# Kernel optimization log

Measured on AMD Instinct MI355X. Metric: run time of the kernel, lower is better.

Reference implementation:

```python
import jax, jax.numpy as jnp
import numpy as np

THRESHOLD = 1e-4


def setup_inputs() -> dict:
    key = jax.random.key(0)
    k1, k2, k3, k4 = jax.random.split(key, 4)
    B, C, T = 512, 128, 1000
    D, O = 64, 4
    X = jax.random.normal(k1, (B, C, T), dtype=jnp.float32)
    # Stiefel-initialized bilinear map W: [1, C, D] with orthonormal columns
    W0 = jax.random.uniform(k2, (1, C, D), dtype=jnp.float32)
    s, U = jnp.linalg.eigh(jnp.swapaxes(W0, -1, -2) @ W0)
    A = (U * jax.lax.rsqrt(jnp.clip(s, THRESHOLD, None))[..., None, :]) @ jnp.swapaxes(U, -1, -2)
    W = W0 @ A
    lin_w = jax.random.normal(k3, (O, D * D), dtype=jnp.float32) / np.sqrt(D * D)
    lin_b = jax.random.normal(k4, (O,), dtype=jnp.float32) * 0.01
    return {"X": X, "W": W, "lin_w": lin_w, "lin_b": lin_b}


def reference(X, W, lin_w, lin_b):
    # CovLayer: per-sample covariance over time axis, correction=0
    T = X.shape[-1]
    Xc = X - jnp.mean(X, axis=-1, keepdims=True)          # [B, C, T]
    Cov = jnp.einsum('bct,bdt->bcd', Xc, Xc) / T           # [B, C, C]
    # BiMap: W^T X W  (W broadcasts over batch)
    Y = jnp.swapaxes(W, -1, -2) @ Cov @ W                  # [B, D, D]
    # ReEig: clamp eigenvalues at threshold, recompose
    s, U = jnp.linalg.eigh(Y)
    s = jnp.clip(s, THRESHOLD, None)
    Y = (U * s[..., None, :]) @ jnp.swapaxes(U, -1, -2)
    # LogEig: log eigenvalues, recompose
    s2, U2 = jnp.linalg.eigh(Y)
    Y = (U2 * jnp.log(s2)[..., None, :]) @ jnp.swapaxes(U2, -1, -2)
    # Flatten + Linear classifier (logsoftmax disabled: add_log_softmax=False)
    F = Y.reshape(Y.shape[0], -1)                          # [B, D*D]
    return F @ lin_w.T + lin_b                             # [B, O]
```

## Files before the change

kernel.cpp:

```cpp
#include <hip/hip_runtime.h>
#include <math.h>

#define NDEG 12

typedef unsigned short u16;
typedef unsigned int u32;
typedef _Float16 f16;
typedef __attribute__((ext_vector_type(8))) _Float16 f16x8;
typedef __attribute__((ext_vector_type(8))) short bf16x8;
typedef __attribute__((ext_vector_type(4))) float f32x4;

#define MFMA_F16(a, b, c)  __builtin_amdgcn_mfma_f32_16x16x32_f16(a, b, c, 0, 0, 0)
#define MFMA_BF16(a, b, c) __builtin_amdgcn_mfma_f32_16x16x32_bf16(a, b, c, 0, 0, 0)

__device__ __forceinline__ u32 fbits(float x) { return __float_as_uint(x); }
__device__ __forceinline__ float fval(u32 u) { return __uint_as_float(u); }
__device__ __forceinline__ f32x4 zero4() {
  f32x4 z; z[0] = 0.f; z[1] = 0.f; z[2] = 0.f; z[3] = 0.f; return z;
}
__device__ __forceinline__ u16 f16bits(f16 x) { u16 u; __builtin_memcpy(&u, &x, 2); return u; }
__device__ __forceinline__ float f16tof(u16 u) { f16 h; __builtin_memcpy(&h, &u, 2); return (float)h; }

__device__ __forceinline__ void split2(float x, u32& h, u32& l) {
  u32 u = fbits(x);
  h = u >> 16;
  float lo = x - fval(u & 0xFFFF0000u);
  u32 v = fbits(lo);
  l = (v + 0x7FFFu + ((v >> 16) & 1u)) >> 16;
}
__device__ __forceinline__ void writePair(u32* Hw, u32* Lw, int widx, float v, int lane) {
  float pv = __shfl_xor(v, 1);
  u32 hv, lv, hp, lp;
  split2(v, hv, lv);
  split2(pv, hp, lp);
  const bool even = (lane & 1) == 0;
  u32 word = even ? (hv | (hp << 16)) : (lp | (lv << 16));
  u32* base = even ? Hw : Lw;
  base[widx] = word;
}

struct CovPh { char buf[3][16384]; };
struct ProjPh { u16 Cov[128][136]; u16 Wt[64][136]; };
struct ChebPh {
  u16 MH[64][72]; u16 ML[64][72];
  u16 TbH[2][64][72]; u16 TbL[2][64][72];
};
struct RedPh { float red[256][4]; };
union SmemU { CovPh a; ProjPh p; ChebPh c; RedPh r; };
static_assert(sizeof(SmemU) <= 65536, "smem");

template <int W, int H>
__device__ __forceinline__ void gram8(const char* bufb, int fo0, int fo1,
                                      f32x4 (&acc)[5], f32x4& xs, f16x8 ones) {
  constexpr int I2 = 7 - W;
#pragma unroll
  for (int ch = 0; ch < 2; ++ch) {
    const int fo = ch ? fo1 : fo0;
    const f16x8 Fi1 = *(const f16x8*)(bufb + W * 2048 + fo);
    const f16x8 Fi2 = *(const f16x8*)(bufb + I2 * 2048 + fo);
    const f16x8 Fxs = *(const f16x8*)(bufb + (2 * W + H) * 2048 + fo);
#pragma unroll
    for (int k = 0; k < 9; ++k) {
      if ((k & 1) != H) continue;
      const int I = (k <= 7 - W) ? W : I2;
      const int J = (k <= 7 - W) ? (W + k) : (I2 + (k - (8 - W)));
      const f16x8 Fj = *(const f16x8*)(bufb + J * 2048 + fo);
      acc[k >> 1] = MFMA_F16((I == W) ? Fi1 : Fi2, Fj, acc[k >> 1]);
    }
    xs = MFMA_F16(Fxs, ones, xs);
  }
}

__device__ __forceinline__ void covTile(u16* Cov, const f32x4& v, int I, int J,
                                        int l15, int l16, bool mirror) {
#pragma unroll
  for (int r = 0; r < 4; ++r) {
    int row = 16 * I + 4 * l16 + r;
    int col = 16 * J + l15;
    u16 h = f16bits((f16)(v[r] * 1e-3f));
    Cov[row * 136 + col] = h;
    if (mirror) Cov[col * 136 + row] = h;
  }
}

template <int W, int H>
__device__ __forceinline__ void covStore8(u16* Cov, const f32x4 (&acc)[5], int l15, int l16) {
  constexpr int I2 = 7 - W;
#pragma unroll
  for (int k = 0; k < 9; ++k) {
    if ((k & 1) != H) continue;
    const int I = (k <= 7 - W) ? W : I2;
    const int J = (k <= 7 - W) ? (W + k) : (I2 + (k - (8 - W)));
    covTile(Cov, acc[k >> 1], I, J, l15, l16, I != J);
  }
}

__global__ __launch_bounds__(512, 4) void spdnet_fused9_kernel(
    const float* __restrict__ X, const float* __restrict__ W,
    const float* __restrict__ lin_w, const float* __restrict__ lin_b,
    float* __restrict__ out)
{
  __shared__ SmemU sm;
  __shared__ float mwL[64];
  __shared__ float xsL[128];

  const int tid = threadIdx.x;
  const int lane = tid & 63;
  const int wv = tid >> 6;
  const int l15 = lane & 15;
  const int l16 = lane >> 4;
  const int b = blockIdx.x;
  const char* __restrict__ Xbc = (const char*)(X + (size_t)b * 128000u);

  int goff[4], lb[4];
#pragma unroll
  for (int q = 0; q < 4; ++q) {
    const int rq = 16 * wv + 4 * q + l16;
    goff[q] = rq * 4000 + l15 * 16;
    lb[q] = rq * 128 + ((l15 * 8) ^ ((rq & 7) << 4));
  }
  const int swz = (l15 & 7) << 4;
  const int fo0 = l15 * 128 + ((16 * l16) ^ swz);
  const int fo1 = l15 * 128 + ((16 * l16 + 64) ^ swz);

  f16x8 ones;
#pragma unroll
  for (int i = 0; i < 8; ++i) ones[i] = (f16)1.0f;

  f32x4 acc[5];
#pragma unroll
  for (int u = 0; u < 5; ++u) acc[u] = zero4();
  f32x4 xs = zero4();

  float4 ldA[4], ldB[4];

#define L4(ld, tile)                                              \
  do {                                                            \
    _Pragma("unroll")                                             \
    for (int q = 0; q < 4; ++q)                                   \
      ld[q] = *(const float4*)(Xbc + goff[q] + (tile) * 256);     \
  } while (0)
#define L4_TAIL(ld)                                               \
  do {                                                            \
    const bool valid = l15 < 10;                                  \
    const int off = valid ? 3840 : (3984 - l15 * 16);             \
    _Pragma("unroll")                                             \
    for (int q = 0; q < 4; ++q) {                                 \
      float4 v = *(const float4*)(Xbc + goff[q] + off);           \
      ld[q] = valid ? v : make_float4(0.f, 0.f, 0.f, 0.f);        \
    }                                                             \
  } while (0)
#define S4(bi, ld)                                                \
  do {                                                            \
    char* rb_ = sm.a.buf[bi];                                     \
    _Pragma("unroll")                                             \
    for (int q = 0; q < 4; ++q) {                                 \
      u32 w0 = (u32)f16bits((f16)ld[q].x) | ((u32)f16bits((f16)ld[q].y) << 16); \
      u32 w1 = (u32)f16bits((f16)ld[q].z) | ((u32)f16bits((f16)ld[q].w) << 16); \
      uint2 wr; wr.x = w0; wr.y = w1;                             \
      *(uint2*)(rb_ + lb[q]) = wr;                                \
    }                                                             \
  } while (0)

  auto GRAM = [&](const char* rb) {
    switch (wv) {
      case 0: gram8<0,0>(rb, fo0, fo1, acc, xs, ones); break;
      case 1: gram8<0,1>(rb, fo0, fo1, acc, xs, ones); break;
      case 2: gram8<1,0>(rb, fo0, fo1, acc, xs, ones); break;
      case 3: gram8<1,1>(rb, fo0, fo1, acc, xs, ones); break;
      case 4: gram8<2,0>(rb, fo0, fo1, acc, xs, ones); break;
      case 5: gram8<2,1>(rb, fo0, fo1, acc, xs, ones); break;
      case 6: gram8<3,0>(rb, fo0, fo1, acc, xs, ones); break;
      default: gram8<3,1>(rb, fo0, fo1, acc, xs, ones); break;
    }
  };

  L4(ldA, 0);
  L4(ldB, 1);
  asm volatile("s_waitcnt vmcnt(4)" ::: "memory");
  S4(0, ldA);
  asm volatile("s_waitcnt lgkmcnt(0)" ::: "memory");
  __builtin_amdgcn_s_barrier();

  for (int h = 0; h < 8; ++h) {
    if (h < 7) L4(ldA, 2 * h + 2);
    GRAM(sm.a.buf[(2 * h) % 3]);
    if (h < 7) asm volatile("s_waitcnt vmcnt(4)" ::: "memory");
    else       asm volatile("s_waitcnt vmcnt(0)" ::: "memory");
    S4((2 * h + 1) % 3, ldB);
    asm volatile("s_waitcnt lgkmcnt(0)" ::: "memory");
    __builtin_amdgcn_s_barrier();
    if (h < 6) L4(ldB, 2 * h + 3);
    else if (h == 6) L4_TAIL(ldB);
    GRAM(sm.a.buf[(2 * h + 1) % 3]);
    if (h < 7) {
      asm volatile("s_waitcnt vmcnt(4)" ::: "memory");
      S4((2 * h + 2) % 3, ldA);
      asm volatile("s_waitcnt lgkmcnt(0)" ::: "memory");
      __builtin_amdgcn_s_barrier();
    }
  }
#undef L4
#undef L4_TAIL
#undef S4

  if (l15 == 0) {
#pragma unroll
    for (int r = 0; r < 4; ++r) xsL[16 * wv + 4 * l16 + r] = xs[r];
  }
  __syncthreads();

  {
    u16* CovP = &sm.p.Cov[0][0];
    switch (wv) {
      case 0: covStore8<0,0>(CovP, acc, l15, l16); break;
      case 1: covStore8<0,1>(CovP, acc, l15, l16); break;
      case 2: covStore8<1,0>(CovP, acc, l15, l16); break;
      case 3: covStore8<1,1>(CovP, acc, l15, l16); break;
      case 4: covStore8<2,0>(CovP, acc, l15, l16); break;
      case 5: covStore8<2,1>(CovP, acc, l15, l16); break;
      case 6: covStore8<3,0>(CovP, acc, l15, l16); break;
      default: covStore8<3,1>(CovP, acc, l15, l16); break;
    }
    u16* WtP = &sm.p.Wt[0][0];
    const int c = tid & 127, dh = tid >> 7;
    const float4* wp = (const float4*)(W + c * 64 + 16 * dh);
#pragma unroll
    for (int q = 0; q < 4; ++q) {
      float4 v = wp[q];
      int d0 = 16 * dh + 4 * q;
      WtP[(d0    ) * 136 + c] = f16bits((f16)v.x);
      WtP[(d0 + 1) * 136 + c] = f16bits((f16)v.y);
      WtP[(d0 + 2) * 136 + c] = f16bits((f16)v.z);
      WtP[(d0 + 3) * 136 + c] = f16bits((f16)v.w);
    }
  }
  __syncthreads();

  if (tid < 64) {
    float s = 0.f;
    for (int c = 0; c < 128; ++c)
      s = fmaf(f16tof(sm.p.Wt[tid][c]), xsL[c], s);
    mwL[tid] = s * 1.0e-3f;
  }

  const u16* CovP = &sm.p.Cov[0][0];
  const u16* WtP  = &sm.p.Wt[0][0];
  f32x4 pAcc[4];
#pragma unroll
  for (int n = 0; n < 4; ++n) pAcc[n] = zero4();
#pragma unroll
  for (int ch = 0; ch < 4; ++ch) {
    f16x8 aC = *(const f16x8*)&CovP[(16 * wv + l15) * 136 + 8 * l16 + 32 * ch];
#pragma unroll
    for (int n = 0; n < 4; ++n) {
      f16x8 bw = *(const f16x8*)&WtP[(16 * n + l15) * 136 + 8 * l16 + 32 * ch];
      pAcc[n] = MFMA_F16(aC, bw, pAcc[n]);
    }
  }
  __syncthreads();

  {
    u16* PtP = (u16*)&sm.p.Cov[0][0];
#pragma unroll
    for (int n = 0; n < 4; ++n)
#pragma unroll
      for (int r = 0; r < 4; ++r) {
        int c = 16 * wv + 4 * l16 + r;
        int d = 16 * n + l15;
        PtP[d * 136 + c] = f16bits((f16)pAcc[n][r]);
      }
  }
  __syncthreads();

  const u16* PtP = (const u16*)&sm.p.Cov[0][0];
  f32x4 yAcc[4];
#pragma unroll
  for (int n = 0; n < 4; ++n) yAcc[n] = zero4();
  if (wv < 4) {
#pragma unroll
    for (int ch = 0; ch < 4; ++ch) {
      f16x8 aW = *(const f16x8*)&WtP[(16 * wv + l15) * 136 + 8 * l16 + 32 * ch];
#pragma unroll
      for (int n = 0; n < 4; ++n) {
        f16x8 bP = *(const f16x8*)&PtP[(16 * n + l15) * 136 + 8 * l16 + 32 * ch];
        yAcc[n] = MFMA_F16(aW, bP, yAcc[n]);
      }
    }
  }
  __syncthreads();

  const float CC = 1.125f;
  const float IH = 1.0f / 0.875f;
  const float uu = 0.875f / 1.125f;
  const float rho = (sqrtf(1.0f - uu * uu) - 1.0f) / uu;
  const float a0c = logf(CC / (1.0f + rho * rho));
  const float a1c = -2.0f * rho;

  f32x4 zz[4], tp[4], tcu[4];
  if (wv < 4) {
    u32* MHw = (u32*)&sm.c.MH[0][0];
    u32* MLw = (u32*)&sm.c.ML[0][0];
#pragma unroll
    for (int n = 0; n < 4; ++n)
#pragma unroll
      for (int r = 0; r < 4; ++r) {
        int i = 16 * wv + 4 * l16 + r, j = 16 * n + l15;
        float y = yAcc[n][r] - mwL[i] * mwL[j];
        float m = (y - ((i == j) ? CC : 0.f)) * IH;
        float e = (i == j) ? 1.f : 0.f;
        tp[n][r] = e;
        tcu[n][r] = m;
        zz[n][r] = a0c * e + a1c * m;
        writePair(MHw, MLw, i * 36 + (j >> 1), m, lane);
      }
  }
  __syncthreads();

  bf16x8 aMh[2], aMl[2];
  if (wv < 4) {
#pragma unroll
    for (int ch = 0; ch < 2; ++ch) {
      aMh[ch] = *(const bf16x8*)&sm.c.MH[16 * wv + l15][8 * l16 + 32 * ch];
      aMl[ch] = *(const bf16x8*)&sm.c.ML[16 * wv + l15][8 * l16 + 32 * ch];
    }
  }

  float rhok = rho;
  for (int k = 2; k <= NDEG; ++k) {
    rhok *= rho;
    const float ak = (-2.0f / (float)k) * rhok;
    if (wv < 4) {
      const u16 (*srcH)[72] = (k == 2) ? sm.c.MH : sm.c.TbH[(k - 1) & 1];
      const u16 (*srcL)[72] = (k == 2) ? sm.c.ML : sm.c.TbL[(k - 1) & 1];
      f32x4 p[4];
#pragma unroll
      for (int n = 0; n < 4; ++n) p[n] = zero4();
#pragma unroll
      for (int ch = 0; ch < 2; ++ch) {
#pragma unroll
        for (int n = 0; n < 4; ++n) {
          bf16x8 bh = *(const bf16x8*)&srcH[16 * n + l15][8 * l16 + 32 * ch];
          bf16x8 bl = *(const bf16x8*)&srcL[16 * n + l15][8 * l16 + 32 * ch];
          p[n] = MFMA_BF16(aMh[ch], bh, p[n]);
          p[n] = MFMA_BF16(aMh[ch], bl, p[n]);
          p[n] = MFMA_BF16(aMl[ch], bh, p[n]);
        }
      }
      u32* dH = (u32*)&sm.c.TbH[k & 1][0][0];
      u32* dL = (u32*)&sm.c.TbL[k & 1][0][0];
#pragma unroll
      for (int n = 0; n < 4; ++n) {
        f32x4 tn;
#pragma unroll
        for (int r = 0; r < 4; ++r) {
          tn[r] = 2.f * p[n][r] - tp[n][r];
          zz[n][r] = fmaf(ak, tn[r], zz[n][r]);
        }
        tp[n] = tcu[n];
        tcu[n] = tn;
        if (k < NDEG) {
#pragma unroll
          for (int r = 0; r < 4; ++r) {
            int row = 16 * wv + 4 * l16 + r, col = 16 * n + l15;
            writePair(dH, dL, row * 36 + (col >> 1), tn[r], lane);
          }
        }
      }
    }
    if (k < NDEG) __syncthreads();
  }
  __syncthreads();

  if (wv < 4) {
    float po[4] = {0.f, 0.f, 0.f, 0.f};
#pragma unroll
    for (int n = 0; n < 4; ++n)
#pragma unroll
      for (int r = 0; r < 4; ++r) {
        int i = 16 * wv + 4 * l16 + r, j = 16 * n + l15;
        const float zv = zz[n][r];
        const int base = i * 64 + j;
#pragma unroll
        for (int o = 0; o < 4; ++o)
          po[o] = fmaf(zv, lin_w[o * 4096 + base], po[o]);
      }
#pragma unroll
    for (int o = 0; o < 4; ++o) sm.r.red[tid][o] = po[o];
  }
  __syncthreads();
  if (tid < 64) {
    const int g = tid >> 4, li = tid & 15;
    float s = 0.f;
#pragma unroll
    for (int q = 0; q < 16; ++q) s += sm.r.red[li + 16 * q][g];
#pragma unroll
    for (int d = 8; d >= 1; d >>= 1) s += __shfl_down(s, d);
    if (li == 0) out[b * 4 + g] = s + lin_b[g];
  }
}

extern "C" void kernel_launch(void* const* d_in, const int* in_sizes, int n_in,
                              void* d_out, int out_size, void* d_ws, size_t ws_size,
                              hipStream_t stream) {
  const float* X     = (const float*)d_in[0];
  const float* W     = (const float*)d_in[1];
  const float* lin_w = (const float*)d_in[2];
  const float* lin_b = (const float*)d_in[3];
  float* out = (float*)d_out;
  spdnet_fused9_kernel<<<512, 512, 0, stream>>>(X, W, lin_w, lin_b, out);
}
```

Baseline: 75.72 us.

## Replace triple-buffered small tiles with single 64KB buffer and large batched loads

The covariance stage previously streamed X in 64-column tiles through a triple-buffered LDS ring, with a barrier per tile. It now loads 256 columns per step into 16 registers per thread, fills one 64KB LDS buffer, and runs four gram passes per barrier pair over four phases. This cuts barrier count and issues larger, more coalesced global loads. In exchange it needs more registers (launch bounds drop to 2 waves per SIMD), and it no longer overlaps the LDS store with compute since the single buffer must be drained before refill.

```diff
diff --git a/kernel.cpp b/kernel.cpp
--- a/kernel.cpp
+++ b/kernel.cpp
@@ -39,7 +39,7 @@
   base[widx] = word;
 }
 
-struct CovPh { char buf[3][16384]; };
+struct CovPh { char buf[65536]; };
 struct ProjPh { u16 Cov[128][136]; u16 Wt[64][136]; };
 struct ChebPh {
   u16 MH[64][72]; u16 ML[64][72];
@@ -47,7 +47,7 @@
 };
 struct RedPh { float red[256][4]; };
 union SmemU { CovPh a; ProjPh p; ChebPh c; RedPh r; };
-static_assert(sizeof(SmemU) <= 65536, "smem");
+static_assert(sizeof(SmemU) == 65536, "smem");
 
 template <int W, int H>
 __device__ __forceinline__ void gram8(const char* bufb, int fo0, int fo1,
@@ -95,7 +95,7 @@
   }
 }
 
-__global__ __launch_bounds__(512, 4) void spdnet_fused9_kernel(
+__global__ __launch_bounds__(512, 2) void spdnet_fused11_kernel(
     const float* __restrict__ X, const float* __restrict__ W,
     const float* __restrict__ lin_w, const float* __restrict__ lin_b,
     float* __restrict__ out)
@@ -112,13 +112,13 @@
   const int b = blockIdx.x;
   const char* __restrict__ Xbc = (const char*)(X + (size_t)b * 128000u);
 
-  int goff[4], lb[4];
-#pragma unroll
-  for (int q = 0; q < 4; ++q) {
-    const int rq = 16 * wv + 4 * q + l16;
-    goff[q] = rq * 4000 + l15 * 16;
-    lb[q] = rq * 128 + ((l15 * 8) ^ ((rq & 7) << 4));
-  }
+  int voff[16];
+#pragma unroll
+  for (int q = 0; q < 16; ++q)
+    voff[q] = (16 * wv + q) * 4000 + lane * 16;
+
+  const int sBase = (lane >> 4) * 16384 + wv * 2048;
+  const int w8 = 8 * (lane & 15);
   const int swz = (l15 & 7) << 4;
   const int fo0 = l15 * 128 + ((16 * l16) ^ swz);
   const int fo1 = l15 * 128 + ((16 * l16 + 64) ^ swz);
@@ -132,77 +132,81 @@
   for (int u = 0; u < 5; ++u) acc[u] = zero4();
   f32x4 xs = zero4();
 
-  float4 ldA[4], ldB[4];
-
-#define L4(ld, tile)                                              \
+  float4 ldA[16];
+
+#define LB(p)                                                     \
   do {                                                            \
     _Pragma("unroll")                                             \
-    for (int q = 0; q < 4; ++q)                                   \
-      ld[q] = *(const float4*)(Xbc + goff[q] + (tile) * 256);     \
+    for (int q = 0; q < 16; ++q)                                  \
+      ldA[q] = *(const float4*)(Xbc + voff[q] + (p) * 1024);      \
   } while (0)
-#define L4_TAIL(ld)                                               \
+#define LB_TAIL()                                                 \
   do {                                                            \
-    const bool valid = l15 < 10;                                  \
-    const int off = valid ? 3840 : (3984 - l15 * 16);             \
+    const bool valid = lane < 58;                                 \
+    const int off = valid ? 3072 : (3984 - 16 * lane);            \
     _Pragma("unroll")                                             \
-    for (int q = 0; q < 4; ++q) {                                 \
-      float4 v = *(const float4*)(Xbc + goff[q] + off);           \
-      ld[q] = valid ? v : make_float4(0.f, 0.f, 0.f, 0.f);        \
+    for (int q = 0; q < 16; ++q) {                                \
+      float4 v = *(const float4*)(Xbc + voff[q] + off);           \
+      ldA[q] = valid ? v : make_float4(0.f, 0.f, 0.f, 0.f);       \
     }                                                             \
   } while (0)
-#define S4(bi, ld)                                                \
+#define SB()                                                      \
   do {                                                            \
-    char* rb_ = sm.a.buf[bi];                                     \
+    char* bb_ = sm.a.buf;                                         \
     _Pragma("unroll")                                             \
-    for (int q = 0; q < 4; ++q) {                                 \
-      u32 w0 = (u32)f16bits((f16)ld[q].x) | ((u32)f16bits((f16)ld[q].y) << 16); \
-      u32 w1 = (u32)f16bits((f16)ld[q].z) | ((u32)f16bits((f16)ld[q].w) << 16); \
+    for (int q = 0; q < 16; ++q) {                                \
+      u32 w0 = (u32)f16bits((f16)ldA[q].x) | ((u32)f16bits((f16)ldA[q].y) << 16); \
+      u32 w1 = (u32)f16bits((f16)ldA[q].z) | ((u32)f16bits((f16)ldA[q].w) << 16); \
       uint2 wr; wr.x = w0; wr.y = w1;                             \
-      *(uint2*)(rb_ + lb[q]) = wr;                                \
+      *(uint2*)(bb_ + sBase + q * 128 + (w8 ^ ((q & 7) << 4))) = wr; \
     }                                                             \
   } while (0)
 
-  auto GRAM = [&](const char* rb) {
+  auto GRAM4 = [&]() {
+    const char* b0 = sm.a.buf;
     switch (wv) {
-      case 0: gram8<0,0>(rb, fo0, fo1, acc, xs, ones); break;
-      case 1: gram8<0,1>(rb, fo0, fo1, acc, xs, ones); break;
-      case 2: gram8<1,0>(rb, fo0, fo1, acc, xs, ones); break;
-      case 3: gram8<1,1>(rb, fo0, fo1, acc, xs, ones); break;
-      case 4: gram8<2,0>(rb, fo0, fo1, acc, xs, ones); break;
-      case 5: gram8<2,1>(rb, fo0, fo1, acc, xs, ones); break;
-      case 6: gram8<3,0>(rb, fo0, fo1, acc, xs, ones); break;
-      default: gram8<3,1>(rb, fo0, fo1, acc, xs, ones); break;
+      case 0: { _Pragma("unroll") for (int s = 0; s < 4; ++s) gram8<0,0>(b0 + s * 16384, fo0, fo1, acc, xs, ones); } break;
+      case 1: { _Pragma("unroll") for (int s = 0; s < 4; ++s) gram8<0,1>(b0 + s * 16384, fo0, fo1, acc, xs, ones); } break;
+      case 2: { _Pragma("unroll") for (int s = 0; s < 4; ++s) gram8<1,0>(b0 + s * 16384, fo0, fo1, acc, xs, ones); } break;
+      case 3: { _Pragma("unroll") for (int s = 0; s < 4; ++s) gram8<1,1>(b0 + s * 16384, fo0, fo1, acc, xs, ones); } break;
+      case 4: { _Pragma("unroll") for (int s = 0; s < 4; ++s) gram8<2,0>(b0 + s * 16384, fo0, fo1, acc, xs, ones); } break;
+      case 5: { _Pragma("unroll") for (int s = 0; s < 4; ++s) gram8<2,1>(b0 + s * 16384, fo0, fo1, acc, xs, ones); } break;
+      case 6: { _Pragma("unroll") for (int s = 0; s < 4; ++s) gram8<3,0>(b0 + s * 16384, fo0, fo1, acc, xs, ones); } break;
+      default:{ _Pragma("unroll") for (int s = 0; s < 4; ++s) gram8<3,1>(b0 + s * 16384, fo0, fo1, acc, xs, ones); } break;
     }
   };
 
-  L4(ldA, 0);
-  L4(ldB, 1);
-  asm volatile("s_waitcnt vmcnt(4)" ::: "memory");
-  S4(0, ldA);
+  LB(0);
+  asm volatile("s_waitcnt vmcnt(0)" ::: "memory");
+  SB();
   asm volatile("s_waitcnt lgkmcnt(0)" ::: "memory");
   __builtin_amdgcn_s_barrier();
 
-  for (int h = 0; h < 8; ++h) {
-    if (h < 7) L4(ldA, 2 * h + 2);
-    GRAM(sm.a.buf[(2 * h) % 3]);
-    if (h < 7) asm volatile("s_waitcnt vmcnt(4)" ::: "memory");
-    else       asm volatile("s_waitcnt vmcnt(0)" ::: "memory");
-    S4((2 * h + 1) % 3, ldB);
-    asm volatile("s_waitcnt lgkmcnt(0)" ::: "memory");
-    __builtin_amdgcn_s_barrier();
-    if (h < 6) L4(ldB, 2 * h + 3);
-    else if (h == 6) L4_TAIL(ldB);
-    GRAM(sm.a.buf[(2 * h + 1) % 3]);
-    if (h < 7) {
-      asm volatile("s_waitcnt vmcnt(4)" ::: "memory");
-      S4((2 * h + 2) % 3, ldA);
-      asm volatile("s_waitcnt lgkmcnt(0)" ::: "memory");
-      __builtin_amdgcn_s_barrier();
-    }
-  }
-#undef L4
-#undef L4_TAIL
-#undef S4
+  LB(1);
+  GRAM4();
+  __builtin_amdgcn_s_barrier();
+  asm volatile("s_waitcnt vmcnt(0)" ::: "memory");
+  SB();
+  asm volatile("s_waitcnt lgkmcnt(0)" ::: "memory");
+  __builtin_amdgcn_s_barrier();
+  LB(2);
+  GRAM4();
+  __builtin_amdgcn_s_barrier();
+  asm volatile("s_waitcnt vmcnt(0)" ::: "memory");
+  SB();
+  asm volatile("s_waitcnt lgkmcnt(0)" ::: "memory");
+  __builtin_amdgcn_s_barrier();
+  LB_TAIL();
+  GRAM4();
+  __builtin_amdgcn_s_barrier();
+  asm volatile("s_waitcnt vmcnt(0)" ::: "memory");
+  SB();
+  asm volatile("s_waitcnt lgkmcnt(0)" ::: "memory");
+  __builtin_amdgcn_s_barrier();
+  GRAM4();
+#undef LB
+#undef LB_TAIL
+#undef SB
 
   if (l15 == 0) {
 #pragma unroll
@@ -408,5 +412,5 @@
   const float* lin_w = (const float*)d_in[2];
   const float* lin_b = (const float*)d_in[3];
   float* out = (float*)d_out;
-  spdnet_fused9_kernel<<<512, 512, 0, stream>>>(X, W, lin_w, lin_b, out);
-}
+  spdnet_fused11_kernel<<<512, 512, 0, stream>>>(X, W, lin_w, lin_b, out);
+}
```

New measurement: 87.63 us. +15.7%, slower.
